# Performance work log

Measured on AMD Instinct MI355X. Metric: run time of the kernel, lower is better.

## Reference

```python
import jax, jax.numpy as jnp
import numpy as np

EPS = 1e-6
INPUT_SIZE = 64
NUM_LEAVES = INPUT_SIZE
NUM_LAYERS = NUM_LEAVES - 1
BATCH = 262144
SINKHORN_ITERS = 20


def _clip01(v):
    return jnp.clip(v, EPS, 1.0 - EPS)


def _F_base(x, y, a, w0, w1):
    # Branches of F for a in [0.5, 2] (the non-recursive region), selected branchlessly.
    x = _clip01(x)
    y = _clip01(y)
    lin = w0 * x + w1 * y
    p = jnp.sqrt(3.0 / jnp.maximum(2.0 - a, EPS)) - 1.0
    g = (x ** (2.0 * w0) * y ** (2.0 * w1)) ** p
    rule0 = jnp.where((jnp.abs(x - 1.0) < EPS) & (jnp.abs(y - 1.0) < EPS), 1.0, 0.0)
    return jnp.where(
        jnp.abs(a - 2.0) < EPS, rule0,
        jnp.where(a >= 0.75, g,
                  jnp.where(a > 0.5, (3.0 - 4.0 * a) * lin + (4.0 * a - 2.0) * g, lin)))


def _F(x, y, a, w0, w1):
    # Full generalized_gcd F with the single-level De Morgan reflection for a < 0.5.
    x = _clip01(x)
    y = _clip01(y)
    hi = _F_base(x, y, a, w0, w1)
    a_ref = jnp.clip(1.0 - a, -1.0 + EPS, 2.0 - EPS)
    lo = 1.0 - _F_base(1.0 - x, 1.0 - y, a_ref, w0, w1)
    lin = w0 * x + w1 * y
    return jnp.where(jnp.abs(a - 0.5) < EPS, lin, jnp.where(a < 0.5, lo, hi))


def _sinkhorn(logits, n_iter=SINKHORN_ITERS):
    # Log-space Sinkhorn normalization -> (approximately) doubly-stochastic P.
    l = logits
    for _ in range(n_iter):
        l = l - jax.nn.logsumexp(l, axis=1, keepdims=True)
        l = l - jax.nn.logsumexp(l, axis=0, keepdims=True)
    return jnp.exp(l)


def setup_inputs() -> dict:
    key = jax.random.key(0)
    k1, k2, k3, k4 = jax.random.split(key, 4)
    x = jax.random.uniform(k1, (BATCH, INPUT_SIZE), dtype=jnp.float32)
    logits = jax.random.normal(k2, (INPUT_SIZE, NUM_LEAVES), dtype=jnp.float32)
    weights = jax.random.uniform(k3, (NUM_LAYERS,), dtype=jnp.float32)
    biases = jax.random.uniform(k4, (NUM_LAYERS,), dtype=jnp.float32)
    return {"x": x, "logits": logits, "weights": weights, "biases": biases}


def reference(x, logits, weights, biases):
    P = _sinkhorn(logits)                 # [INPUT_SIZE, NUM_LEAVES], columns sum to 1
    leaves = (x @ P).T                    # [NUM_LEAVES, BATCH]

    def step(carry, inp):
        leaf, w, b = inp
        nres = _F(carry, leaf, b, w, 1.0 - w)
        nres = jnp.where(jnp.isnan(nres), b, nres)  # NaN fallback to bias, as in torch forward
        return nres, None

    # Left-leaning tree: state_0 = leaf_0; state_i = F(state_{i-1}, leaf_i, b, w, 1-w)
    final, _ = jax.lax.scan(step, leaves[0], (leaves[1:], weights, biases))
    return final[:, None]                 # [BATCH, 1]
```

## Files before the change

kernel.cpp:

```cpp
#include <hip/hip_runtime.h>
#include <hip/hip_bf16.h>
#include <math.h>

#define EPS 1e-6f
#define NLAYERS 63
#define SINK_ITERS 20
#define LOG2E 1.4426950408889634f

typedef __attribute__((ext_vector_type(8))) short bf16x8;
typedef __attribute__((ext_vector_type(4))) float f32x4;
typedef __attribute__((ext_vector_type(4))) unsigned int ui32x4;

__device__ __forceinline__ float fast_log2(float v) {
#if __has_builtin(__builtin_amdgcn_logf)
  return __builtin_amdgcn_logf(v);
#else
  return log2f(v);
#endif
}
__device__ __forceinline__ float fast_exp2(float v) {
#if __has_builtin(__builtin_amdgcn_exp2f)
  return __builtin_amdgcn_exp2f(v);
#else
  return exp2f(v);
#endif
}

__device__ __forceinline__ unsigned int f2bf(float f) {
  unsigned int u = __float_as_uint(f);
  return (u + 0x7FFFu + ((u >> 16) & 1u)) >> 16;
}

__device__ __forceinline__ unsigned int cvt_pk_bf16(float lo, float hi) {
  unsigned int r;
  asm("v_cvt_pk_bf16_f32 %0, %1, %2" : "=v"(r) : "v"(lo), "v"(hi));
  return r;
}
__device__ __forceinline__ bf16x8 pack8(float4 a, float4 b) {
  ui32x4 u;
  u[0] = cvt_pk_bf16(a.x, a.y);
  u[1] = cvt_pk_bf16(a.z, a.w);
  u[2] = cvt_pk_bf16(b.x, b.y);
  u[3] = cvt_pk_bf16(b.z, b.w);
  return __builtin_bit_cast(bf16x8, u);
}


__global__ __launch_bounds__(256) void sinkhorn_kernel(
    const float* __restrict__ logits,
    const float* __restrict__ weights,
    const float* __restrict__ biases,
    unsigned short* __restrict__ Pfrag,
    float* __restrict__ layers) {
  __shared__ float T[64 * 65];
  __shared__ float Uv[64];
  __shared__ float Vv[64];
  __shared__ float part[256];

  const int tid = threadIdx.x;
  const int w = tid >> 6, l = tid & 63;
  const int q = l >> 4, c = l & 15;

  if (tid < NLAYERS) {
    float w0 = weights[tid];
    float w1 = 1.0f - w0;
    float a  = biases[tid];
    float sgn, e0, e1, cw0, cw1, lcg;
    if (fabsf(a - 0.5f) < EPS) {
      sgn = 1.f; e0 = 0.f; e1 = 0.f; cw0 = w0; cw1 = w1; lcg = -1.0e30f;
    } else {
      float ae;
      if (a < 0.5f) { sgn = -1.f; ae = fminf(fmaxf(1.0f - a, -1.0f + EPS), 2.0f - EPS); }
      else          { sgn =  1.f; ae = a; }
      float pp = sqrtf(3.0f / fmaxf(2.0f - ae, EPS)) - 1.0f;
      float cl, cg;
      if (ae >= 0.75f) { cl = 0.0f;            cg = 1.0f; }
      else             { cl = 3.0f - 4.0f*ae;  cg = 4.0f*ae - 2.0f; }
      e0  = 2.0f * w0 * pp;
      e1  = 2.0f * w1 * pp;
      cw0 = cl * w0;
      cw1 = cl * w1;
      lcg = (cg > 0.f) ? log2f(cg) : -1.0e30f;
    }
    float sgnp = 1.f;
    if (tid > 0) {
      float ap = biases[tid - 1];
      sgnp = (fabsf(ap - 0.5f) < EPS) ? 1.f : (ap < 0.5f ? -1.f : 1.f);
    }
    float Sc = sgn * sgnp;
    float Oc = 0.5f - 0.5f * Sc;
    float* Lr = layers + tid * 8;
    Lr[0] = sgn; Lr[1] = e1; Lr[2] = lcg; Lr[3] = cw1;
    Lr[4] = Sc;  Lr[5] = Oc; Lr[6] = e0;  Lr[7] = cw0;
  }

  float K_part[16], KT_part[16];
  {
    const float4* lr = (const float4*)(logits + (l << 6) + (w << 4));
    #pragma unroll
    for (int i = 0; i < 4; ++i) {
      float4 t = lr[i];
      K_part[4*i+0] = fast_exp2(t.x * LOG2E);
      K_part[4*i+1] = fast_exp2(t.y * LOG2E);
      K_part[4*i+2] = fast_exp2(t.z * LOG2E);
      K_part[4*i+3] = fast_exp2(t.w * LOG2E);
    }
  }
  #pragma unroll
  for (int i = 0; i < 16; ++i) T[l * 65 + (w << 4) + i] = K_part[i];
  if (tid < 64) Vv[tid] = 1.0f;
  __syncthreads();
  #pragma unroll
  for (int i = 0; i < 16; ++i) KT_part[i] = T[((w << 4) + i) * 65 + l];

  for (int it = 0; it < SINK_ITERS; ++it) {
    float p0 = 0.f, p1 = 0.f, p2 = 0.f, p3 = 0.f;
    #pragma unroll
    for (int i = 0; i < 4; ++i) {
      p0 = fmaf(K_part[4*i+0], Vv[(w << 4) + 4*i+0], p0);
      p1 = fmaf(K_part[4*i+1], Vv[(w << 4) + 4*i+1], p1);
      p2 = fmaf(K_part[4*i+2], Vv[(w << 4) + 4*i+2], p2);
      p3 = fmaf(K_part[4*i+3], Vv[(w << 4) + 4*i+3], p3);
    }
    part[(w << 6) + l] = (p0 + p1) + (p2 + p3);
    __syncthreads();
    if (tid < 64) {
      float s = (part[tid] + part[64 + tid]) + (part[128 + tid] + part[192 + tid]);
      Uv[tid] = 1.0f / s;
    }
    __syncthreads();
    float q0 = 0.f, q1 = 0.f, q2 = 0.f, q3 = 0.f;
    #pragma unroll
    for (int i = 0; i < 4; ++i) {
      q0 = fmaf(KT_part[4*i+0], Uv[(w << 4) + 4*i+0], q0);
      q1 = fmaf(KT_part[4*i+1], Uv[(w << 4) + 4*i+1], q1);
      q2 = fmaf(KT_part[4*i+2], Uv[(w << 4) + 4*i+2], q2);
      q3 = fmaf(KT_part[4*i+3], Uv[(w << 4) + 4*i+3], q3);
    }
    part[(w << 6) + l] = (q0 + q1) + (q2 + q3);
    __syncthreads();
    if (tid < 64) {
      float s = (part[tid] + part[64 + tid]) + (part[128 + tid] + part[192 + tid]);
      Vv[tid] = 1.0f / s;
    }
    __syncthreads();
  }

  {
    const float ul = Uv[l];
    #pragma unroll
    for (int i = 0; i < 16; ++i)
      T[l * 65 + (w << 4) + i] = ul * K_part[i] * Vv[(w << 4) + i];
  }
  __syncthreads();

  #pragma unroll
  for (int fi = 0; fi < 2; ++fi) {
    const int f = (w << 1) + fi;
    const int s = f >> 2, t = f & 3;
    ui32x4 u;
    #pragma unroll
    for (int jj = 0; jj < 4; ++jj) {
      unsigned int lo = f2bf(T[(s*32 + (q << 3) + 2*jj    ) * 65 + t*16 + c]);
      unsigned int hi = f2bf(T[(s*32 + (q << 3) + 2*jj + 1) * 65 + t*16 + c]);
      u[jj] = lo | (hi << 16);
    }
    *(ui32x4*)(Pfrag + ((f * 64 + l) << 3)) = u;
  }
}


template<int HALF>
__device__ __forceinline__ void do_gemm(const bf16x8 (&Bf)[2][4],
                                        const bf16x8 (&Af)[4][2],
                                        float* Lv, int w, int q, int c) {
  #pragma unroll
  for (int rt = 0; rt < 4; ++rt) {
    #pragma unroll
    for (int lt = 0; lt < 2; ++lt) {
      f32x4 acc = {0.f, 0.f, 0.f, 0.f};
      acc = __builtin_amdgcn_mfma_f32_16x16x32_bf16(Bf[0][(HALF << 1) + lt], Af[rt][0], acc, 0, 0, 0);
      acc = __builtin_amdgcn_mfma_f32_16x16x32_bf16(Bf[1][(HALF << 1) + lt], Af[rt][1], acc, 0, 0, 0);
      const int row  = (w << 6) + (rt << 4) + c;
      const int nloc = (lt << 4) + (q << 2);
      *(f32x4*)&Lv[row * 36 + nloc] = acc;
    }
  }
}

template<int L0>
__device__ __forceinline__ void do_chunk(const float* Lrow,
                                         const float4* Lp4, float& r) {
  constexpr int loc = L0 & 31;
  f32x4 lf0 = *(const f32x4*)&Lrow[loc];
  f32x4 lf1 = *(const f32x4*)&Lrow[loc + 4];
  float lf[8] = {lf0[0], lf0[1], lf0[2], lf0[3], lf1[0], lf1[1], lf1[2], lf1[3]};

  float ylin[8], ylg[8];
  #pragma unroll
  for (int k = 0; k < 8; ++k) {
    if (L0 + k >= 1) {
      float4 p0 = Lp4[(L0 + k - 1) * 2];
      float off = fmaf(-0.5f, p0.x, 0.5f);
      float yy  = fminf(fmaxf(lf[k], EPS), 1.0f - EPS);
      float yr  = fmaf(p0.x, yy, off);
      float ly  = fast_log2(yr);
      ylg[k]  = fmaf(p0.y, ly, p0.z);
      ylin[k] = p0.w * yr;
    }
  }

  #pragma unroll
  for (int k = 0; k < 8; ++k) {
    if (L0 + k >= 1) {
      float4 p1 = Lp4[(L0 + k - 1) * 2 + 1];
      float cr = fminf(fmaxf(r, EPS), 1.0f - EPS);
      float xr = fmaf(p1.x, cr, p1.y);
      float lx = fast_log2(xr);
      float g  = fast_exp2(fmaf(p1.z, lx, ylg[k]));
      r = fmaf(p1.w, xr, ylin[k]) + g;
    } else {
      r = lf[0];
    }
  }
}

__global__ __launch_bounds__(256, 4) void scan_kernel(
    const float* __restrict__ x,
    const unsigned short* __restrict__ Pfrag,
    const float* __restrict__ layers,
    float* __restrict__ out) {
  __shared__ float Lv[256 * 36];
  const int tid = threadIdx.x;
  const int w = tid >> 6, l = tid & 63;
  const int q = l >> 4, c = l & 15;
  const size_t rowbase = (size_t)blockIdx.x << 8;
  const float4* Lp4 = (const float4*)layers;

  bf16x8 Af[4][2];
  {
    const float* rp0 = x + (rowbase + (w << 6) + c) * 64 + (q << 3);
    float4 t0[4], t1[4];
    #define LOADROW(dst, i) do {                                   \
      const float* rp = rp0 + ((i) << 4) * 64;                     \
      (dst)[0] = *(const float4*)(rp);                             \
      (dst)[1] = *(const float4*)(rp + 4);                         \
      (dst)[2] = *(const float4*)(rp + 32);                        \
      (dst)[3] = *(const float4*)(rp + 36);                        \
    } while (0)
    LOADROW(t0, 0);
    LOADROW(t1, 1);
    Af[0][0] = pack8(t0[0], t0[1]); Af[0][1] = pack8(t0[2], t0[3]);
    LOADROW(t0, 2);
    Af[1][0] = pack8(t1[0], t1[1]); Af[1][1] = pack8(t1[2], t1[3]);
    LOADROW(t1, 3);
    Af[2][0] = pack8(t0[0], t0[1]); Af[2][1] = pack8(t0[2], t0[3]);
    Af[3][0] = pack8(t1[0], t1[1]); Af[3][1] = pack8(t1[2], t1[3]);
    #undef LOADROW
  }

  bf16x8 Bf[2][4];
  #pragma unroll
  for (int s = 0; s < 2; ++s)
    #pragma unroll
    for (int t = 0; t < 4; ++t)
      Bf[s][t] = *(const bf16x8*)(Pfrag + (((s*4 + t) * 64 + l) << 3));

  const float* Lrow = &Lv[tid * 36];
  float r = 0.f;

  do_gemm<0>(Bf, Af, Lv, w, q, c);
  do_chunk<0>(Lrow, Lp4, r);
  do_chunk<8>(Lrow, Lp4, r);
  do_chunk<16>(Lrow, Lp4, r);
  do_chunk<24>(Lrow, Lp4, r);

  do_gemm<1>(Bf, Af, Lv, w, q, c);
  do_chunk<32>(Lrow, Lp4, r);
  do_chunk<40>(Lrow, Lp4, r);
  do_chunk<48>(Lrow, Lp4, r);
  do_chunk<56>(Lrow, Lp4, r);

  const float sgnL = layers[62 * 8];
  out[rowbase + tid] = fmaf(sgnL, r, fmaf(-0.5f, sgnL, 0.5f));
}

extern "C" void kernel_launch(void* const* d_in, const int* in_sizes, int n_in,
                              void* d_out, int out_size, void* d_ws, size_t ws_size,
                              hipStream_t stream) {
  const float* x       = (const float*)d_in[0];
  const float* logits  = (const float*)d_in[1];
  const float* weights = (const float*)d_in[2];
  const float* biases  = (const float*)d_in[3];
  float* out = (float*)d_out;

  unsigned short* Pfrag = (unsigned short*)d_ws;
  float* layers = (float*)((char*)d_ws + 8 * 64 * 8 * sizeof(unsigned short));

  const int batch = out_size;

  hipLaunchKernelGGL(sinkhorn_kernel, dim3(1), dim3(256), 0, stream,
                     logits, weights, biases, Pfrag, layers);
  hipLaunchKernelGGL(scan_kernel, dim3(batch / 256), dim3(256), 0, stream,
                     x, Pfrag, layers, out);
}
```

Measured before the change: 115.4 us.

## Process two row tiles per block, prefetching the second tile during the first scan

Each block now handles 512 rows in two passes of 256. The x loads for the second tile are issued right after the first GEMM, so their latency overlaps the first tile's scan. The P fragments are loaded once and reused across both passes. The kernel drops its occupancy hint from 4 to 2 blocks per CU, because holding 64 float prefetch registers raises register pressure. The grid is halved, which risks lower occupancy hurting the latency hiding of the transcendental-heavy scan.

```diff
diff --git a/kernel.cpp b/kernel.cpp
--- a/kernel.cpp
+++ b/kernel.cpp
@@ -225,7 +225,33 @@
   }
 }
 
-__global__ __launch_bounds__(256, 4) void scan_kernel(
+__device__ __forceinline__ void run_pass(const bf16x8 (&Bf)[2][4],
+                                         const bf16x8 (&Af)[4][2],
+                                         float* Lv, const float4* Lp4,
+                                         const float* __restrict__ layers,
+                                         float* __restrict__ out,
+                                         size_t rowbase, int tid,
+                                         int w, int q, int c) {
+  const float* Lrow = &Lv[tid * 36];
+  float r = 0.f;
+
+  do_gemm<0>(Bf, Af, Lv, w, q, c);
+  do_chunk<0>(Lrow, Lp4, r);
+  do_chunk<8>(Lrow, Lp4, r);
+  do_chunk<16>(Lrow, Lp4, r);
+  do_chunk<24>(Lrow, Lp4, r);
+
+  do_gemm<1>(Bf, Af, Lv, w, q, c);
+  do_chunk<32>(Lrow, Lp4, r);
+  do_chunk<40>(Lrow, Lp4, r);
+  do_chunk<48>(Lrow, Lp4, r);
+  do_chunk<56>(Lrow, Lp4, r);
+
+  const float sgnL = layers[62 * 8];
+  out[rowbase + tid] = fmaf(sgnL, r, fmaf(-0.5f, sgnL, 0.5f));
+}
+
+__global__ __launch_bounds__(256, 2) void scan_kernel(
     const float* __restrict__ x,
     const unsigned short* __restrict__ Pfrag,
     const float* __restrict__ layers,
@@ -234,29 +260,31 @@
   const int tid = threadIdx.x;
   const int w = tid >> 6, l = tid & 63;
   const int q = l >> 4, c = l & 15;
-  const size_t rowbase = (size_t)blockIdx.x << 8;
+  const size_t rowbase = (size_t)blockIdx.x << 9;
   const float4* Lp4 = (const float4*)layers;
 
-  bf16x8 Af[4][2];
+  const float* rpA = x + (rowbase + (w << 6) + c) * 64 + (q << 3);
+  const float* rpB = rpA + 256 * 64;
+
+  #define LOADROW(dst, base, i) do {                               \
+    const float* rp = (base) + ((i) << 4) * 64;                    \
+    (dst)[0] = *(const float4*)(rp);                               \
+    (dst)[1] = *(const float4*)(rp + 4);                           \
+    (dst)[2] = *(const float4*)(rp + 32);                          \
+    (dst)[3] = *(const float4*)(rp + 36);                          \
+  } while (0)
+
+  bf16x8 AfA[4][2];
   {
-    const float* rp0 = x + (rowbase + (w << 6) + c) * 64 + (q << 3);
     float4 t0[4], t1[4];
-    #define LOADROW(dst, i) do {                                   \
-      const float* rp = rp0 + ((i) << 4) * 64;                     \
-      (dst)[0] = *(const float4*)(rp);                             \
-      (dst)[1] = *(const float4*)(rp + 4);                         \
-      (dst)[2] = *(const float4*)(rp + 32);                        \
-      (dst)[3] = *(const float4*)(rp + 36);                        \
-    } while (0)
-    LOADROW(t0, 0);
-    LOADROW(t1, 1);
-    Af[0][0] = pack8(t0[0], t0[1]); Af[0][1] = pack8(t0[2], t0[3]);
-    LOADROW(t0, 2);
-    Af[1][0] = pack8(t1[0], t1[1]); Af[1][1] = pack8(t1[2], t1[3]);
-    LOADROW(t1, 3);
-    Af[2][0] = pack8(t0[0], t0[1]); Af[2][1] = pack8(t0[2], t0[3]);
-    Af[3][0] = pack8(t1[0], t1[1]); Af[3][1] = pack8(t1[2], t1[3]);
-    #undef LOADROW
+    LOADROW(t0, rpA, 0);
+    LOADROW(t1, rpA, 1);
+    AfA[0][0] = pack8(t0[0], t0[1]); AfA[0][1] = pack8(t0[2], t0[3]);
+    LOADROW(t0, rpA, 2);
+    AfA[1][0] = pack8(t1[0], t1[1]); AfA[1][1] = pack8(t1[2], t1[3]);
+    LOADROW(t1, rpA, 3);
+    AfA[2][0] = pack8(t0[0], t0[1]); AfA[2][1] = pack8(t0[2], t0[3]);
+    AfA[3][0] = pack8(t1[0], t1[1]); AfA[3][1] = pack8(t1[2], t1[3]);
   }
 
   bf16x8 Bf[2][4];
@@ -266,23 +294,37 @@
     for (int t = 0; t < 4; ++t)
       Bf[s][t] = *(const bf16x8*)(Pfrag + (((s*4 + t) * 64 + l) << 3));
 
-  const float* Lrow = &Lv[tid * 36];
-  float r = 0.f;
-
-  do_gemm<0>(Bf, Af, Lv, w, q, c);
-  do_chunk<0>(Lrow, Lp4, r);
-  do_chunk<8>(Lrow, Lp4, r);
-  do_chunk<16>(Lrow, Lp4, r);
-  do_chunk<24>(Lrow, Lp4, r);
-
-  do_gemm<1>(Bf, Af, Lv, w, q, c);
-  do_chunk<32>(Lrow, Lp4, r);
-  do_chunk<40>(Lrow, Lp4, r);
-  do_chunk<48>(Lrow, Lp4, r);
-  do_chunk<56>(Lrow, Lp4, r);
+  const float* LrowA = &Lv[tid * 36];
+  float rA = 0.f;
+
+  do_gemm<0>(Bf, AfA, Lv, w, q, c);
+
+  float4 xb[4][4];
+  #pragma unroll
+  for (int i = 0; i < 4; ++i)
+    LOADROW(xb[i], rpB, i);
+  #undef LOADROW
+
+  do_chunk<0>(LrowA, Lp4, rA);
+  do_chunk<8>(LrowA, Lp4, rA);
+  do_chunk<16>(LrowA, Lp4, rA);
+  do_chunk<24>(LrowA, Lp4, rA);
+  do_gemm<1>(Bf, AfA, Lv, w, q, c);
+  do_chunk<32>(LrowA, Lp4, rA);
+  do_chunk<40>(LrowA, Lp4, rA);
+  do_chunk<48>(LrowA, Lp4, rA);
+  do_chunk<56>(LrowA, Lp4, rA);
 
   const float sgnL = layers[62 * 8];
-  out[rowbase + tid] = fmaf(sgnL, r, fmaf(-0.5f, sgnL, 0.5f));
+  out[rowbase + tid] = fmaf(sgnL, rA, fmaf(-0.5f, sgnL, 0.5f));
+
+  bf16x8 AfB[4][2];
+  #pragma unroll
+  for (int i = 0; i < 4; ++i) {
+    AfB[i][0] = pack8(xb[i][0], xb[i][1]);
+    AfB[i][1] = pack8(xb[i][2], xb[i][3]);
+  }
+  run_pass(Bf, AfB, Lv, Lp4, layers, out, rowbase + 256, tid, w, q, c);
 }
 
 extern "C" void kernel_launch(void* const* d_in, const int* in_sizes, int n_in,
@@ -301,6 +343,6 @@
 
   hipLaunchKernelGGL(sinkhorn_kernel, dim3(1), dim3(256), 0, stream,
                      logits, weights, biases, Pfrag, layers);
-  hipLaunchKernelGGL(scan_kernel, dim3(batch / 256), dim3(256), 0, stream,
+  hipLaunchKernelGGL(scan_kernel, dim3(batch / 512), dim3(256), 0, stream,
                      x, Pfrag, layers, out);
 }
```

New measurement: 123.3 us. +6.8%, slower.
